# Kernel optimization log

Hardware: AMD Instinct MI355X
Metric: run time of the kernel (lower is better)

## Reference

```python
import jax, jax.numpy as jnp
import numpy as np
from jax import lax

B, C_E, C_D, H, W, K = 64, 768, 512, 28, 28, 3
EPS = 1e-6


def setup_inputs() -> dict:
    key = jax.random.key(0)
    k1, k2, k3, k4, k5 = jax.random.split(key, 5)
    bcff = jax.random.normal(k1, (B, C_E, H, W), dtype=jnp.float32)
    cur_active = jax.random.bernoulli(k2, p=0.25, shape=(B, 1, H, W))
    # learned mask token, trunc-normal(std=0.02)
    mask_token = jnp.clip(0.02 * jax.random.normal(k3, (1, C_E, 1, 1), dtype=jnp.float32), -0.02, 0.02)
    ln_weight = jnp.ones((C_E,), dtype=jnp.float32)
    ln_bias = jnp.zeros((C_E,), dtype=jnp.float32)
    fan_in = C_E * K * K
    bound = 1.0 / np.sqrt(fan_in)
    conv_w = jax.random.uniform(k4, (C_D, C_E, K, K), minval=-bound, maxval=bound, dtype=jnp.float32)
    conv_b = jax.random.uniform(k5, (C_D,), minval=-bound, maxval=bound, dtype=jnp.float32)
    return {"bcff": bcff, "cur_active": cur_active, "mask_token": mask_token,
            "ln_weight": ln_weight, "ln_bias": ln_bias, "conv_w": conv_w, "conv_b": conv_b}


def reference(bcff, cur_active, mask_token, ln_weight, ln_bias, conv_w, conv_b):
    # Sparse channels-first LayerNorm: per-position LN over C. Original gathers
    # active positions, LNs them, scatters back into zeros. Since inactive
    # positions are subsequently replaced by mask tokens via torch.where, the
    # dense-LN-then-where form below is mathematically identical.
    mu = jnp.mean(bcff, axis=1, keepdims=True)                      # [B,1,H,W]
    var = jnp.mean((bcff - mu) ** 2, axis=1, keepdims=True)         # biased var, like torch LN
    normed = (bcff - mu) * lax.rsqrt(var + EPS)
    normed = ln_weight[None, :, None, None] * normed + ln_bias[None, :, None, None]
    # masked token fill: active positions keep normed features, inactive get mask token
    x = jnp.where(cur_active, normed, mask_token)                   # [B,C_E,H,W]
    # densify_proj: 3x3 conv, stride 1, padding 1, with bias
    y = lax.conv_general_dilated(x, conv_w, window_strides=(1, 1), padding="SAME",
                                 dimension_numbers=("NCHW", "OIHW", "NCHW"))
    return y + conv_b[None, :, None, None]
```

## Files before the change

### kernel.cpp

```cpp
#include <hip/hip_runtime.h>
#include <cstdint>
#include <cstddef>

#define CE 768
#define CD 512
#define NB 64
#define HH 28
#define WW 28
#define HP 30
#define WP 30
#define POS 784
#define M_TOT 50176
#define K_TOT 6912
#define MP 57600
#define XP_PIX 57728

typedef _Float16 f16x8 __attribute__((ext_vector_type(8)));
typedef _Float16 f16x4 __attribute__((ext_vector_type(4)));
typedef float f32x4 __attribute__((ext_vector_type(4)));

__global__ void prep_w_kernel(const float* __restrict__ cw, _Float16* __restrict__ wT) {
  __shared__ _Float16 s[K_TOT];
  int co = blockIdx.x;
  const float4* src4 = (const float4*)(cw + (size_t)co * K_TOT);
  for (int j = threadIdx.x; j < K_TOT / 4; j += 256) {
    float4 v = src4[j];
    f16x4 o = { (_Float16)v.x, (_Float16)v.y, (_Float16)v.z, (_Float16)v.w };
    *(f16x4*)&s[j * 4] = o;
  }
  __syncthreads();
  _Float16* dst = wT + (size_t)co * K_TOT;
  for (int j4 = threadIdx.x; j4 < K_TOT / 4; j4 += 256) {
    int tap = j4 / 192;
    int ci0 = (j4 - tap * 192) * 4;
    f16x4 o = { s[(ci0 + 0) * 9 + tap], s[(ci0 + 1) * 9 + tap],
                s[(ci0 + 2) * 9 + tap], s[(ci0 + 3) * 9 + tap] };
    *(f16x4*)&dst[j4 * 4] = o;
  }
}

__global__ void __launch_bounds__(512) ln_fused_kernel(
    const float* __restrict__ bcff, const int* __restrict__ act,
    const float* __restrict__ mtok, const float* __restrict__ gamma,
    const float* __restrict__ beta, _Float16* __restrict__ xp) {
  int b = blockIdx.x / HP, ph = blockIdx.x % HP;
  _Float16* xrow = xp + ((size_t)(b * HP + ph)) * WP * CE;
  const int tid = threadIdx.x;
  if (ph == 0 || ph == HP - 1) {
    uint4* p = (uint4*)xrow;
    uint4 z = make_uint4(0, 0, 0, 0);
    for (int j = tid; j < (WP * CE * 2) / 16; j += 512) p[j] = z;
    return;
  }
  int h = ph - 1;
  {
    uint4 z = make_uint4(0, 0, 0, 0);
    uint4* p0 = (uint4*)xrow;
    uint4* p1 = (uint4*)(xrow + (size_t)(WP - 1) * CE);
    for (int j = tid; j < (CE * 2) / 16; j += 512) { p0[j] = z; p1[j] = z; }
  }

  __shared__ _Float16 tile[WW][776];
  __shared__ float s_gamma[CE], s_beta[CE];
  __shared__ _Float16 s_mt[CE];
  __shared__ float s_mean[WW], s_rstd[WW];
  __shared__ int s_act[WW];

  for (int c = tid; c < CE; c += 512) {
    s_gamma[c] = gamma[c];
    s_beta[c] = beta[c];
    s_mt[c] = (_Float16)mtok[c];
  }
  if (tid < WW) s_act[tid] = act[b * POS + h * WW + tid];

  const float4* src4 = (const float4*)(bcff + ((size_t)b * CE * HH + h) * WW);
  for (int i = tid; i < 1344; i += 512) {
    int cq = i / 7, w4 = i - cq * 7;
    int c0 = cq * 4;
    float4 v0 = src4[(size_t)(c0 + 0) * 196 + w4];
    float4 v1 = src4[(size_t)(c0 + 1) * 196 + w4];
    float4 v2 = src4[(size_t)(c0 + 2) * 196 + w4];
    float4 v3 = src4[(size_t)(c0 + 3) * 196 + w4];
    f16x4 o0 = { (_Float16)v0.x, (_Float16)v1.x, (_Float16)v2.x, (_Float16)v3.x };
    f16x4 o1 = { (_Float16)v0.y, (_Float16)v1.y, (_Float16)v2.y, (_Float16)v3.y };
    f16x4 o2 = { (_Float16)v0.z, (_Float16)v1.z, (_Float16)v2.z, (_Float16)v3.z };
    f16x4 o3 = { (_Float16)v0.w, (_Float16)v1.w, (_Float16)v2.w, (_Float16)v3.w };
    *(f16x4*)&tile[w4 * 4 + 0][c0] = o0;
    *(f16x4*)&tile[w4 * 4 + 1][c0] = o1;
    *(f16x4*)&tile[w4 * 4 + 2][c0] = o2;
    *(f16x4*)&tile[w4 * 4 + 3][c0] = o3;
  }
  __syncthreads();

  if (tid < WW * 16) {
    int w = tid >> 4, j = tid & 15;
    float s = 0.f, ss = 0.f;
    const _Float16* row = &tile[w][j * 48];
#pragma unroll
    for (int k = 0; k < 6; ++k) {
      f16x8 v = *(const f16x8*)(row + k * 8);
#pragma unroll
      for (int u = 0; u < 8; ++u) { float f = (float)v[u]; s += f; ss += f * f; }
    }
#pragma unroll
    for (int d = 8; d; d >>= 1) {
      s += __shfl_down(s, d, 16);
      ss += __shfl_down(ss, d, 16);
    }
    if (j == 0) {
      float mu = s * (1.f / 768.f);
      float var = ss * (1.f / 768.f) - mu * mu;
      s_mean[w] = mu;
      s_rstd[w] = rsqrtf(var + 1e-6f);
    }
  }
  __syncthreads();

  for (int i = tid; i < WW * 96; i += 512) {
    int w = i / 96, q = i - w * 96;
    int c0 = q * 8;
    f16x8 o;
    if (s_act[w]) {
      f16x8 v = *(const f16x8*)&tile[w][c0];
      float mu = s_mean[w], rs = s_rstd[w];
#pragma unroll
      for (int u = 0; u < 8; ++u)
        o[u] = (_Float16)(((float)v[u] - mu) * rs * s_gamma[c0 + u] + s_beta[c0 + u]);
    } else {
      o = *(const f16x8*)&s_mt[c0];
    }
    *(f16x8*)(xrow + (size_t)(w + 1) * CE + c0) = o;
  }
}

#define GLDS(src, dst) __builtin_amdgcn_global_load_lds( \
    (const __attribute__((address_space(1))) void*)(src), \
    (__attribute__((address_space(3))) void*)(dst), 16, 0, 0)

__global__ void __launch_bounds__(512) conv_strip_kernel(
    const _Float16* __restrict__ xp, const _Float16* __restrict__ wT,
    const float* __restrict__ bias, float* __restrict__ out) {
  __shared__ _Float16 smem[47104];
  char* sAb = (char*)smem;
  char* sBb = sAb + 20480;

  const int t = threadIdx.x;
  const int lane = t & 63, wv = t >> 6;
  const int nb = blockIdx.x & 3;
  const int mb = blockIdx.x >> 2;
  const int p0 = mb * 256;
  const int n0 = nb * 128;

  const int jj = (t & 3) ^ ((t >> 3) & 3);
  const int pixA = t >> 2;
  const _Float16* pA = xp + (size_t)(p0 + pixA) * CE + jj * 8;
  const int colB = t >> 2;
  const _Float16* pB = wT + (size_t)(n0 + colB) * K_TOT + jj * 8;
  char* dA = sAb + t * 16;
  char* dB = sBb + t * 16;

  const int wm = wv >> 1, wn = wv & 1;
  const int lq = lane >> 4;
  const int l15 = lane & 15;
  const int rowbase0 = wm * 64 + l15;
  const int bbase = (wn * 64 + l15) * 64 + ((lq ^ ((l15 >> 1) & 3)) * 16);

  f32x4 acc[4][4] = {};
  const int tap_off[9] = {0, 1, 2, 30, 31, 32, 60, 61, 62};

  for (int c24 = 0; c24 < 24; ++c24) {
    const int koff = c24 * 32;
    GLDS(pA + koff, dA);
    GLDS(pA + (size_t)128 * CE + koff, dA + 8192);
    if (t < 256) GLDS(pA + (size_t)256 * CE + koff, dA + 16384);
#pragma unroll
    for (int k = 0; k < 9; ++k)
      GLDS(pB + k * CE + koff, dB + 8192 * k);
    __syncthreads();

#pragma unroll
    for (int tap = 0; tap < 9; ++tap) {
      const int rA = rowbase0 + tap_off[tap];
      f16x8 a[4], b[4];
#pragma unroll
      for (int mi = 0; mi < 4; ++mi) {
        const int r = rA + mi * 16;
        a[mi] = *(const f16x8*)(sAb + r * 64 + ((lq ^ ((r >> 1) & 3)) * 16));
      }
      const char* bp = sBb + tap * 8192 + bbase;
#pragma unroll
      for (int ni = 0; ni < 4; ++ni)
        b[ni] = *(const f16x8*)(bp + ni * 1024);
#pragma unroll
      for (int mi = 0; mi < 4; ++mi)
#pragma unroll
        for (int ni = 0; ni < 4; ++ni)
          acc[mi][ni] = __builtin_amdgcn_mfma_f32_16x16x32_f16(a[mi], b[ni], acc[mi][ni], 0, 0, 0);
    }
    __syncthreads();
  }

  float bv[4];
#pragma unroll
  for (int ni = 0; ni < 4; ++ni) bv[ni] = bias[n0 + wn * 64 + ni * 16 + l15];
#pragma unroll
  for (int mi = 0; mi < 4; ++mi) {
    int g = p0 + wm * 64 + mi * 16 + lq * 4;
    int b = g / 900;
    int q = g - b * 900;
    int ph = q / 30, pw = q - ph * 30;
#pragma unroll
    for (int ni = 0; ni < 4; ++ni) {
      int co = n0 + wn * 64 + ni * 16 + l15;
      f32x4 v = acc[mi][ni];
      v += bv[ni];
      float* obase = out + ((size_t)b * CD + co) * POS;
      if (b < NB && ph < 28) {
        if (pw <= 24) {
          *(f32x4*)(obase + ph * 28 + pw) = v;
        } else if (pw == 26) {
          obase[ph * 28 + 26] = v[0];
          obase[ph * 28 + 27] = v[1];
        }
      }
      if (pw == 28) {
        int b2 = b, ph2 = ph + 1;
        if (ph2 == 30) { b2++; ph2 = 0; }
        if (b2 < NB && ph2 < 28) {
          float* o2 = out + ((size_t)b2 * CD + co) * POS + ph2 * 28;
          o2[0] = v[2];
          o2[1] = v[3];
        }
      }
    }
  }
}

extern "C" void kernel_launch(void* const* d_in, const int* in_sizes, int n_in,
                              void* d_out, int out_size, void* d_ws, size_t ws_size,
                              hipStream_t stream) {
  const float* bcff = (const float*)d_in[0];
  const int* cur_active = (const int*)d_in[1];
  const float* mask_token = (const float*)d_in[2];
  const float* ln_w = (const float*)d_in[3];
  const float* ln_b = (const float*)d_in[4];
  const float* conv_w = (const float*)d_in[5];
  const float* conv_b = (const float*)d_in[6];
  float* out = (float*)d_out;

  char* ws = (char*)d_ws;
  _Float16* xp = (_Float16*)ws;
  _Float16* wT = (_Float16*)(ws + (size_t)XP_PIX * CE * 2);

  prep_w_kernel<<<dim3(CD), dim3(256), 0, stream>>>(conv_w, wT);
  ln_fused_kernel<<<dim3(NB * HP), dim3(512), 0, stream>>>(bcff, cur_active, mask_token,
                                                           ln_w, ln_b, xp);
  conv_strip_kernel<<<dim3(225 * 4), dim3(512), 0, stream>>>(xp, wT, conv_b, out);
}
```

Measured before the change: 704.1 us.

## Double-buffer conv K-chunks in LDS and switch to 32x32x16 MFMA tiles

Rewrites the implicit-GEMM conv main loop to use 16-wide K chunks, 48 iterations in total, with two LDS buffers. Global-to-LDS loads of the next chunk are issued while MFMAs run on the current one, which removes the exposed load latency between the two barriers of the old loop. Each wave now uses 2x2 tiles of 32x32x16 MFMA instead of 4x4 tiles of 16x16x32, which needs fewer LDS fragment reads per flop. The LDS swizzle changes to an 8-way XOR, and the epilogue is adapted to the 32x32 accumulator layout. LDS use roughly doubles to about 94KB per block, which may cut occupancy.

```diff
diff --git a/kernel.cpp b/kernel.cpp
--- a/kernel.cpp
+++ b/kernel.cpp
@@ -18,6 +18,7 @@
 typedef _Float16 f16x8 __attribute__((ext_vector_type(8)));
 typedef _Float16 f16x4 __attribute__((ext_vector_type(4)));
 typedef float f32x4 __attribute__((ext_vector_type(4)));
+typedef float f32x16 __attribute__((ext_vector_type(16)));
 
 __global__ void prep_w_kernel(const float* __restrict__ cw, _Float16* __restrict__ wT) {
   __shared__ _Float16 s[K_TOT];
@@ -137,103 +138,134 @@
     (const __attribute__((address_space(1))) void*)(src), \
     (__attribute__((address_space(3))) void*)(dst), 16, 0, 0)
 
+#define BM 256
+#define BN 128
+#define AROWS 320
+#define ABYTES 10240
+#define BBYTES 36864
+#define BUFB 47104
+#define NCH 48
+
 __global__ void __launch_bounds__(512) conv_strip_kernel(
     const _Float16* __restrict__ xp, const _Float16* __restrict__ wT,
     const float* __restrict__ bias, float* __restrict__ out) {
-  __shared__ _Float16 smem[47104];
-  char* sAb = (char*)smem;
-  char* sBb = sAb + 20480;
+  __shared__ __align__(16) char smem[2 * BUFB];
 
   const int t = threadIdx.x;
   const int lane = t & 63, wv = t >> 6;
   const int nb = blockIdx.x & 3;
   const int mb = blockIdx.x >> 2;
-  const int p0 = mb * 256;
-  const int n0 = nb * 128;
-
-  const int jj = (t & 3) ^ ((t >> 3) & 3);
-  const int pixA = t >> 2;
-  const _Float16* pA = xp + (size_t)(p0 + pixA) * CE + jj * 8;
-  const int colB = t >> 2;
-  const _Float16* pB = wT + (size_t)(n0 + colB) * K_TOT + jj * 8;
-  char* dA = sAb + t * 16;
-  char* dB = sBb + t * 16;
+  const int p0 = mb * BM;
+  const int n0 = nb * BN;
+
+  const int lsA0 = t ^ ((t >> 3) & 7);
+  const int sA1 = 512 + t;
+  const int lsA1 = sA1 ^ ((sA1 >> 3) & 7);
+  const _Float16* pa0 = xp + (size_t)(p0 + (lsA0 >> 1)) * CE + (lsA0 & 1) * 8;
+  const _Float16* pa1 = xp + (size_t)(p0 + (lsA1 >> 1)) * CE + (lsA1 & 1) * 8;
+  const _Float16* pb0; const _Float16* pb1; const _Float16* pb2;
+  const _Float16* pb3; const _Float16* pb4;
+  {
+    int s, ls;
+    s = t;                 ls = s ^ ((s >> 3) & 7);
+    pb0 = wT + (size_t)(n0 + ((ls & 255) >> 1)) * K_TOT + (ls >> 8) * 768 + (ls & 1) * 8;
+    s = 512 + t;           ls = s ^ ((s >> 3) & 7);
+    pb1 = wT + (size_t)(n0 + ((ls & 255) >> 1)) * K_TOT + (ls >> 8) * 768 + (ls & 1) * 8;
+    s = 1024 + t;          ls = s ^ ((s >> 3) & 7);
+    pb2 = wT + (size_t)(n0 + ((ls & 255) >> 1)) * K_TOT + (ls >> 8) * 768 + (ls & 1) * 8;
+    s = 1536 + t;          ls = s ^ ((s >> 3) & 7);
+    pb3 = wT + (size_t)(n0 + ((ls & 255) >> 1)) * K_TOT + (ls >> 8) * 768 + (ls & 1) * 8;
+    s = 2048 + (t & 255);  ls = s ^ ((s >> 3) & 7);
+    pb4 = wT + (size_t)(n0 + ((ls & 255) >> 1)) * K_TOT + (ls >> 8) * 768 + (ls & 1) * 8;
+  }
 
   const int wm = wv >> 1, wn = wv & 1;
-  const int lq = lane >> 4;
-  const int l15 = lane & 15;
-  const int rowbase0 = wm * 64 + l15;
-  const int bbase = (wn * 64 + l15) * 64 + ((lq ^ ((l15 >> 1) & 3)) * 16);
-
-  f32x4 acc[4][4] = {};
+  const int l31 = lane & 31, kh = lane >> 5;
   const int tap_off[9] = {0, 1, 2, 30, 31, 32, 60, 61, 62};
-
-  for (int c24 = 0; c24 < 24; ++c24) {
-    const int koff = c24 * 32;
-    GLDS(pA + koff, dA);
-    GLDS(pA + (size_t)128 * CE + koff, dA + 8192);
-    if (t < 256) GLDS(pA + (size_t)256 * CE + koff, dA + 16384);
-#pragma unroll
-    for (int k = 0; k < 9; ++k)
-      GLDS(pB + k * CE + koff, dB + 8192 * k);
+  int offA[9];
+#pragma unroll
+  for (int tap = 0; tap < 9; ++tap) {
+    int u = (wm * 64 + l31 + tap_off[tap]) * 2 + kh;
+    offA[tap] = (u ^ ((u >> 3) & 7)) * 16;
+  }
+  int offB;
+  {
+    int u = (wn * 64 + l31) * 2 + kh;
+    offB = ABYTES + ((u ^ ((u >> 3) & 7)) * 16);
+  }
+
+  f32x16 acc[2][2] = {};
+
+#define STAGE(wb, c) do { \
+    GLDS(pa0 + (c) * 16, (wb) + t * 16); \
+    if (wv < 2) GLDS(pa1 + (c) * 16, (wb) + 8192 + t * 16); \
+    GLDS(pb0 + (c) * 16, (wb) + ABYTES + t * 16); \
+    GLDS(pb1 + (c) * 16, (wb) + ABYTES + 8192 + t * 16); \
+    GLDS(pb2 + (c) * 16, (wb) + ABYTES + 16384 + t * 16); \
+    GLDS(pb3 + (c) * 16, (wb) + ABYTES + 24576 + t * 16); \
+    if (wv < 4) GLDS(pb4 + (c) * 16, (wb) + ABYTES + 32768 + t * 16); \
+  } while (0)
+
+  STAGE((char*)smem, 0);
+  __syncthreads();
+
+  for (int c = 0; c < NCH; ++c) {
+    char* rb = (char*)smem + (c & 1) * BUFB;
+    char* wb = (char*)smem + ((c & 1) ^ 1) * BUFB;
+    if (c + 1 < NCH) STAGE(wb, c + 1);
+#pragma unroll
+    for (int tap = 0; tap < 9; ++tap) {
+      f16x8 a0 = *(const f16x8*)(rb + offA[tap]);
+      f16x8 a1 = *(const f16x8*)(rb + offA[tap] + 1024);
+      f16x8 b0 = *(const f16x8*)(rb + offB + tap * 4096);
+      f16x8 b1 = *(const f16x8*)(rb + offB + tap * 4096 + 1024);
+      acc[0][0] = __builtin_amdgcn_mfma_f32_32x32x16_f16(a0, b0, acc[0][0], 0, 0, 0);
+      acc[0][1] = __builtin_amdgcn_mfma_f32_32x32x16_f16(a0, b1, acc[0][1], 0, 0, 0);
+      acc[1][0] = __builtin_amdgcn_mfma_f32_32x32x16_f16(a1, b0, acc[1][0], 0, 0, 0);
+      acc[1][1] = __builtin_amdgcn_mfma_f32_32x32x16_f16(a1, b1, acc[1][1], 0, 0, 0);
+    }
     __syncthreads();
-
-#pragma unroll
-    for (int tap = 0; tap < 9; ++tap) {
-      const int rA = rowbase0 + tap_off[tap];
-      f16x8 a[4], b[4];
-#pragma unroll
-      for (int mi = 0; mi < 4; ++mi) {
-        const int r = rA + mi * 16;
-        a[mi] = *(const f16x8*)(sAb + r * 64 + ((lq ^ ((r >> 1) & 3)) * 16));
-      }
-      const char* bp = sBb + tap * 8192 + bbase;
-#pragma unroll
-      for (int ni = 0; ni < 4; ++ni)
-        b[ni] = *(const f16x8*)(bp + ni * 1024);
-#pragma unroll
-      for (int mi = 0; mi < 4; ++mi)
-#pragma unroll
-        for (int ni = 0; ni < 4; ++ni)
-          acc[mi][ni] = __builtin_amdgcn_mfma_f32_16x16x32_f16(a[mi], b[ni], acc[mi][ni], 0, 0, 0);
-    }
-    __syncthreads();
-  }
-
-  float bv[4];
-#pragma unroll
-  for (int ni = 0; ni < 4; ++ni) bv[ni] = bias[n0 + wn * 64 + ni * 16 + l15];
-#pragma unroll
-  for (int mi = 0; mi < 4; ++mi) {
-    int g = p0 + wm * 64 + mi * 16 + lq * 4;
-    int b = g / 900;
-    int q = g - b * 900;
-    int ph = q / 30, pw = q - ph * 30;
-#pragma unroll
-    for (int ni = 0; ni < 4; ++ni) {
-      int co = n0 + wn * 64 + ni * 16 + l15;
-      f32x4 v = acc[mi][ni];
-      v += bv[ni];
-      float* obase = out + ((size_t)b * CD + co) * POS;
-      if (b < NB && ph < 28) {
-        if (pw <= 24) {
-          *(f32x4*)(obase + ph * 28 + pw) = v;
-        } else if (pw == 26) {
-          obase[ph * 28 + 26] = v[0];
-          obase[ph * 28 + 27] = v[1];
+  }
+
+  float bv[2];
+#pragma unroll
+  for (int ni = 0; ni < 2; ++ni) bv[ni] = bias[n0 + wn * 64 + ni * 32 + l31];
+#pragma unroll
+  for (int mi = 0; mi < 2; ++mi) {
+#pragma unroll
+    for (int g = 0; g < 4; ++g) {
+      int p = p0 + wm * 64 + mi * 32 + kh * 4 + g * 8;
+      int b = p / 900;
+      int q = p - b * 900;
+      int ph = q / 30, pw = q - ph * 30;
+#pragma unroll
+      for (int ni = 0; ni < 2; ++ni) {
+        int co = n0 + wn * 64 + ni * 32 + l31;
+        f32x4 v = { acc[mi][ni][g * 4 + 0], acc[mi][ni][g * 4 + 1],
+                    acc[mi][ni][g * 4 + 2], acc[mi][ni][g * 4 + 3] };
+        v += bv[ni];
+        float* obase = out + ((size_t)b * CD + co) * POS;
+        if (b < NB && ph < 28) {
+          if (pw <= 24) {
+            *(f32x4*)(obase + ph * 28 + pw) = v;
+          } else if (pw == 26) {
+            obase[ph * 28 + 26] = v[0];
+            obase[ph * 28 + 27] = v[1];
+          }
+        }
+        if (pw == 28) {
+          int b2 = b, ph2 = ph + 1;
+          if (ph2 == 30) { b2++; ph2 = 0; }
+          if (b2 < NB && ph2 < 28) {
+            float* o2 = out + ((size_t)b2 * CD + co) * POS + ph2 * 28;
+            o2[0] = v[2];
+            o2[1] = v[3];
+          }
         }
       }
-      if (pw == 28) {
-        int b2 = b, ph2 = ph + 1;
-        if (ph2 == 30) { b2++; ph2 = 0; }
-        if (b2 < NB && ph2 < 28) {
-          float* o2 = out + ((size_t)b2 * CD + co) * POS + ph2 * 28;
-          o2[0] = v[2];
-          o2[1] = v[3];
-        }
-      }
-    }
-  }
+    }
+  }
+#undef STAGE
 }
 
 extern "C" void kernel_launch(void* const* d_in, const int* in_sizes, int n_in,
```

New measurement: 732.0 us. 1.04x slower.
